# Optimization experiments

Hardware: AMD Instinct MI355X
Metric: run time of the kernel (lower is better)

The kernel has to match this reference:

```python
import jax, jax.numpy as jnp
import numpy as np

B, S, E, F = 64, 8192, 8, 32  # batch, seq, embed_dim(=n_qubits), ffn_dim


def setup_inputs() -> dict:
    key = jax.random.key(0)
    k_x, k_t, k_w1, k_b1, k_w2, k_b2 = jax.random.split(key, 6)
    x = jax.random.normal(k_x, (B, S, E), dtype=jnp.float32)
    theta = jax.random.normal(k_t, (E,), dtype=jnp.float32)  # trainable RX angles
    lim1 = 1.0 / np.sqrt(E)
    lim2 = 1.0 / np.sqrt(F)
    w1 = jax.random.uniform(k_w1, (E, F), jnp.float32, -lim1, lim1)
    b1 = jax.random.uniform(k_b1, (F,), jnp.float32, -lim1, lim1)
    w2 = jax.random.uniform(k_w2, (F, E), jnp.float32, -lim2, lim2)
    b2 = jax.random.uniform(k_b2, (E,), jnp.float32, -lim2, lim2)
    return {"x": x, "theta": theta, "w1": w1, "b1": b1, "w2": w2, "b2": b2}


def reference(x, theta, w1, b1, w2, b2):
    # Quantum circuit: per wire i, RX(x_i) then RX(theta_i) on |0>, measure PauliZ.
    # Single-qubit RX gates compose: <Z> after RX(phi)|0> = cos(phi). Wires are
    # independent (no entangling gates), so MeasureAll(PauliZ) = cos(x + theta).
    q_out = jnp.cos(x + theta)                      # [B, S, E]
    h = jax.nn.relu(q_out @ w1 + b1)                # [B, S, F]
    return h @ w2 + b2                              # [B, S, E]
```

## Files before the change

kernel.cpp:

```cpp
#include <hip/hip_runtime.h>


#define TPB 256

typedef _Float16 h8 __attribute__((ext_vector_type(8)));
typedef __fp16   fp16x2 __attribute__((ext_vector_type(2)));
typedef float    f4 __attribute__((ext_vector_type(4)));

union H2I { fp16x2 h; int i; };
union I4H8 { int i[4]; h8 h; };

__device__ __forceinline__ int pack_f16(float a, float b) {
    H2I u;
    u.h = __builtin_amdgcn_cvt_pkrtz(a, b);
    return u.i;
}

__global__ __launch_bounds__(TPB) void ffq_kernel(
    const float4* __restrict__ xv,
    const float*  __restrict__ theta,
    const float*  __restrict__ w1,
    const float*  __restrict__ b1,
    const float*  __restrict__ w2,
    const float*  __restrict__ b2,
    float4*       __restrict__ outv,
    int ntile, int nwaves)
{
    const int tid  = threadIdx.x;
    const int lane = tid & 63;
    const int widx = tid >> 6;
    const int quad = lane >> 4;
    const int m16  = lane & 15;

    h8 a1lo, a1hi, a2;
#pragma unroll
    for (int j = 0; j < 8; ++j) { a1lo[j] = (_Float16)0; a1hi[j] = (_Float16)0; a2[j] = (_Float16)0; }

    if (quad == 0) {
#pragma unroll
        for (int j = 0; j < 8; ++j) {
            a1lo[j] = (_Float16)w1[j * 32 + m16];
            a1hi[j] = (_Float16)w1[j * 32 + 16 + m16];
        }
    }
    if (m16 < 8) {
#pragma unroll
        for (int j = 0; j < 8; ++j)
            a2[j] = (_Float16)w2[(quad * 8 + j) * 8 + m16];
    }

    f4 c1lo0, c1hi0, c20;
#pragma unroll
    for (int r = 0; r < 4; ++r) {
        c1lo0[r] = b1[quad * 4 + r];
        c1hi0[r] = b1[16 + quad * 4 + r];
        c20[r]   = (quad < 2) ? b2[quad * 4 + r] : 0.0f;
    }

    float th[8];
#pragma unroll
    for (int e = 0; e < 8; ++e) th[e] = theta[e];

    const int addr0 = (((2 * quad) & 3) * 16 + m16) * 4;
    const int addr1 = (((2 * quad + 1) & 3) * 16 + m16) * 4;

    const int wid = blockIdx.x * (TPB / 64) + widx;

    float4 curA = make_float4(0.f, 0.f, 0.f, 0.f);
    float4 curC = curA;
    if (wid < ntile && lane < 16) {
        const int tok = wid * 16 + lane;
        curA = xv[2 * tok];
        curC = xv[2 * tok + 1];
    }

    for (int tile = wid; tile < ntile; tile += nwaves) {
        float4 nA = curA, nC = curC;
        const int nxt = tile + nwaves;
        if (nxt < ntile && lane < 16) {
            const int tok = nxt * 16 + lane;
            nA = xv[2 * tok];
            nC = xv[2 * tok + 1];
        }

        h8 bq;
#pragma unroll
        for (int j = 0; j < 8; ++j) bq[j] = (_Float16)0;
        if (lane < 16) {
            bq[0] = (_Float16)__cosf(curA.x + th[0]);
            bq[1] = (_Float16)__cosf(curA.y + th[1]);
            bq[2] = (_Float16)__cosf(curA.z + th[2]);
            bq[3] = (_Float16)__cosf(curA.w + th[3]);
            bq[4] = (_Float16)__cosf(curC.x + th[4]);
            bq[5] = (_Float16)__cosf(curC.y + th[5]);
            bq[6] = (_Float16)__cosf(curC.z + th[6]);
            bq[7] = (_Float16)__cosf(curC.w + th[7]);
        }

        f4 c1lo = __builtin_amdgcn_mfma_f32_16x16x32_f16(a1lo, bq, c1lo0, 0, 0, 0);
        f4 c1hi = __builtin_amdgcn_mfma_f32_16x16x32_f16(a1hi, bq, c1hi0, 0, 0, 0);

#pragma unroll
        for (int r = 0; r < 4; ++r) {
            c1lo[r] = fmaxf(c1lo[r], 0.0f);
            c1hi[r] = fmaxf(c1hi[r], 0.0f);
        }

        const int lo01 = pack_f16(c1lo[0], c1lo[1]);
        const int lo23 = pack_f16(c1lo[2], c1lo[3]);
        const int hi01 = pack_f16(c1hi[0], c1hi[1]);
        const int hi23 = pack_f16(c1hi[2], c1hi[3]);

        const int tL0 = __builtin_amdgcn_ds_bpermute(addr0, lo01);
        const int tL1 = __builtin_amdgcn_ds_bpermute(addr0, lo23);
        const int tL2 = __builtin_amdgcn_ds_bpermute(addr1, lo01);
        const int tL3 = __builtin_amdgcn_ds_bpermute(addr1, lo23);
        const int tH0 = __builtin_amdgcn_ds_bpermute(addr0, hi01);
        const int tH1 = __builtin_amdgcn_ds_bpermute(addr0, hi23);
        const int tH2 = __builtin_amdgcn_ds_bpermute(addr1, hi01);
        const int tH3 = __builtin_amdgcn_ds_bpermute(addr1, hi23);

        I4H8 bh;
        bh.i[0] = (quad < 2) ? tL0 : tH0;
        bh.i[1] = (quad < 2) ? tL1 : tH1;
        bh.i[2] = (quad < 2) ? tL2 : tH2;
        bh.i[3] = (quad < 2) ? tL3 : tH3;

        f4 o = __builtin_amdgcn_mfma_f32_16x16x32_f16(a2, bh.h, c20, 0, 0, 0);

        if (quad < 2) {
            const int tok = tile * 16 + m16;
            outv[2 * tok + quad] = make_float4(o[0], o[1], o[2], o[3]);
        }

        curA = nA; curC = nC;
    }
}

extern "C" void kernel_launch(void* const* d_in, const int* in_sizes, int n_in,
                              void* d_out, int out_size, void* d_ws, size_t ws_size,
                              hipStream_t stream) {
    const float* x     = (const float*)d_in[0];
    const float* theta = (const float*)d_in[1];
    const float* w1    = (const float*)d_in[2];
    const float* b1    = (const float*)d_in[3];
    const float* w2    = (const float*)d_in[4];
    const float* b2    = (const float*)d_in[5];
    float* out = (float*)d_out;

    const int ntok  = in_sizes[0] / 8;
    const int ntile = ntok / 16;
    const int grid  = 1024;
    const int nwaves = grid * (TPB / 64);

    ffq_kernel<<<grid, TPB, 0, stream>>>(
        (const float4*)x, theta, w1, b1, w2, b2, (float4*)out, ntile, nwaves);
}
```

Baseline: 81.27 us.

## Use 32x32x16 MFMA for first layer and LDS transpose for 32-token tiles

Tiles grow from 16 to 32 tokens per wave. The first FFN layer becomes a single 32x32x16 MFMA in place of two 16x16x32 MFMAs, and the hidden activations are reshuffled through padded LDS writes and reads instead of ds_bpermute, feeding two 16x16x32 MFMAs for the second layer. This halves the loop iterations and the per-token MFMA issue count, but adds LDS stores and loads per tile and still leaves half the lanes idle during the cos and load phase.

```diff
diff --git a/kernel.cpp b/kernel.cpp
--- a/kernel.cpp
+++ b/kernel.cpp
@@ -3,9 +3,10 @@
 
 #define TPB 256
 
-typedef _Float16 h8 __attribute__((ext_vector_type(8)));
+typedef _Float16 h8  __attribute__((ext_vector_type(8)));
 typedef __fp16   fp16x2 __attribute__((ext_vector_type(2)));
-typedef float    f4 __attribute__((ext_vector_type(4)));
+typedef float    f4  __attribute__((ext_vector_type(4)));
+typedef float    f16v __attribute__((ext_vector_type(16)));
 
 union H2I { fp16x2 h; int i; };
 union I4H8 { int i[4]; h8 h; };
@@ -26,50 +27,47 @@
     float4*       __restrict__ outv,
     int ntile, int nwaves)
 {
+    __shared__ int lds[4 * 576];
+
     const int tid  = threadIdx.x;
     const int lane = tid & 63;
     const int widx = tid >> 6;
-    const int quad = lane >> 4;
+    const int half = lane >> 5;
+    const int l31  = lane & 31;
+    const int quad = (lane >> 4) & 3;
     const int m16  = lane & 15;
 
-    h8 a1lo, a1hi, a2;
+    h8 a1;
 #pragma unroll
-    for (int j = 0; j < 8; ++j) { a1lo[j] = (_Float16)0; a1hi[j] = (_Float16)0; a2[j] = (_Float16)0; }
+    for (int j = 0; j < 8; ++j)
+        a1[j] = (half == 0) ? (_Float16)w1[j * 32 + l31] : (_Float16)0;
 
-    if (quad == 0) {
+    h8 a2;
 #pragma unroll
-        for (int j = 0; j < 8; ++j) {
-            a1lo[j] = (_Float16)w1[j * 32 + m16];
-            a1hi[j] = (_Float16)w1[j * 32 + 16 + m16];
-        }
-    }
-    if (m16 < 8) {
+    for (int j = 0; j < 8; ++j)
+        a2[j] = (m16 < 8) ? (_Float16)w2[(quad * 8 + j) * 8 + m16] : (_Float16)0;
+
+    f16v c10;
 #pragma unroll
-        for (int j = 0; j < 8; ++j)
-            a2[j] = (_Float16)w2[(quad * 8 + j) * 8 + m16];
-    }
+    for (int r = 0; r < 16; ++r)
+        c10[r] = b1[(r & 3) + 8 * (r >> 2) + 4 * half];
 
-    f4 c1lo0, c1hi0, c20;
+    f4 c20;
 #pragma unroll
-    for (int r = 0; r < 4; ++r) {
-        c1lo0[r] = b1[quad * 4 + r];
-        c1hi0[r] = b1[16 + quad * 4 + r];
-        c20[r]   = (quad < 2) ? b2[quad * 4 + r] : 0.0f;
-    }
+    for (int r = 0; r < 4; ++r)
+        c20[r] = (quad < 2) ? b2[quad * 4 + r] : 0.0f;
 
     float th[8];
 #pragma unroll
     for (int e = 0; e < 8; ++e) th[e] = theta[e];
 
-    const int addr0 = (((2 * quad) & 3) * 16 + m16) * 4;
-    const int addr1 = (((2 * quad + 1) & 3) * 16 + m16) * 4;
-
+    const int base_w = widx * 576;
     const int wid = blockIdx.x * (TPB / 64) + widx;
 
     float4 curA = make_float4(0.f, 0.f, 0.f, 0.f);
     float4 curC = curA;
-    if (wid < ntile && lane < 16) {
-        const int tok = wid * 16 + lane;
+    if (wid < ntile && half == 0) {
+        const int tok = wid * 32 + l31;
         curA = xv[2 * tok];
         curC = xv[2 * tok + 1];
     }
@@ -77,8 +75,8 @@
     for (int tile = wid; tile < ntile; tile += nwaves) {
         float4 nA = curA, nC = curC;
         const int nxt = tile + nwaves;
-        if (nxt < ntile && lane < 16) {
-            const int tok = nxt * 16 + lane;
+        if (nxt < ntile && half == 0) {
+            const int tok = nxt * 32 + l31;
             nA = xv[2 * tok];
             nC = xv[2 * tok + 1];
         }
@@ -86,7 +84,7 @@
         h8 bq;
 #pragma unroll
         for (int j = 0; j < 8; ++j) bq[j] = (_Float16)0;
-        if (lane < 16) {
+        if (half == 0) {
             bq[0] = (_Float16)__cosf(curA.x + th[0]);
             bq[1] = (_Float16)__cosf(curA.y + th[1]);
             bq[2] = (_Float16)__cosf(curA.z + th[2]);
@@ -97,40 +95,32 @@
             bq[7] = (_Float16)__cosf(curC.w + th[7]);
         }
 
-        f4 c1lo = __builtin_amdgcn_mfma_f32_16x16x32_f16(a1lo, bq, c1lo0, 0, 0, 0);
-        f4 c1hi = __builtin_amdgcn_mfma_f32_16x16x32_f16(a1hi, bq, c1hi0, 0, 0, 0);
+        f16v c1 = __builtin_amdgcn_mfma_f32_32x32x16_f16(a1, bq, c10, 0, 0, 0);
 
 #pragma unroll
-        for (int r = 0; r < 4; ++r) {
-            c1lo[r] = fmaxf(c1lo[r], 0.0f);
-            c1hi[r] = fmaxf(c1hi[r], 0.0f);
-        }
+        for (int r = 0; r < 16; ++r) c1[r] = fmaxf(c1[r], 0.0f);
+        int pk[8];
+#pragma unroll
+        for (int i = 0; i < 8; ++i) pk[i] = pack_f16(c1[2 * i], c1[2 * i + 1]);
 
-        const int lo01 = pack_f16(c1lo[0], c1lo[1]);
-        const int lo23 = pack_f16(c1lo[2], c1lo[3]);
-        const int hi01 = pack_f16(c1hi[0], c1hi[1]);
-        const int hi23 = pack_f16(c1hi[2], c1hi[3]);
+#pragma unroll
+        for (int i = 0; i < 8; ++i)
+            lds[base_w + lane * 9 + i] = pk[i];
 
-        const int tL0 = __builtin_amdgcn_ds_bpermute(addr0, lo01);
-        const int tL1 = __builtin_amdgcn_ds_bpermute(addr0, lo23);
-        const int tL2 = __builtin_amdgcn_ds_bpermute(addr1, lo01);
-        const int tL3 = __builtin_amdgcn_ds_bpermute(addr1, lo23);
-        const int tH0 = __builtin_amdgcn_ds_bpermute(addr0, hi01);
-        const int tH1 = __builtin_amdgcn_ds_bpermute(addr0, hi23);
-        const int tH2 = __builtin_amdgcn_ds_bpermute(addr1, hi01);
-        const int tH3 = __builtin_amdgcn_ds_bpermute(addr1, hi23);
+#pragma unroll
+        for (int tg = 0; tg < 2; ++tg) {
+            I4H8 bh;
+#pragma unroll
+            for (int p = 0; p < 4; ++p)
+                bh.i[p] = lds[base_w + (32 * (p >> 1) + 16 * tg + m16) * 9
+                              + 2 * quad + (p & 1)];
 
-        I4H8 bh;
-        bh.i[0] = (quad < 2) ? tL0 : tH0;
-        bh.i[1] = (quad < 2) ? tL1 : tH1;
-        bh.i[2] = (quad < 2) ? tL2 : tH2;
-        bh.i[3] = (quad < 2) ? tL3 : tH3;
+            f4 o = __builtin_amdgcn_mfma_f32_16x16x32_f16(a2, bh.h, c20, 0, 0, 0);
 
-        f4 o = __builtin_amdgcn_mfma_f32_16x16x32_f16(a2, bh.h, c20, 0, 0, 0);
-
-        if (quad < 2) {
-            const int tok = tile * 16 + m16;
-            outv[2 * tok + quad] = make_float4(o[0], o[1], o[2], o[3]);
+            if (quad < 2) {
+                const int tok = tile * 32 + 16 * tg + m16;
+                outv[2 * tok + quad] = make_float4(o[0], o[1], o[2], o[3]);
+            }
         }
 
         curA = nA; curC = nC;
@@ -149,7 +139,7 @@
     float* out = (float*)d_out;
 
     const int ntok  = in_sizes[0] / 8;
-    const int ntile = ntok / 16;
+    const int ntile = ntok / 32;
     const int grid  = 1024;
     const int nwaves = grid * (TPB / 64);
 
```

Measured after the change: 80.83 us. No clear change (-0.5%).
